# Kernel tuning notes

Measured on AMD Instinct MI355X. Metric: run time of the kernel, lower is better.

The kernel has to match this reference:

```python
import jax, jax.numpy as jnp
import numpy as np

_SAMPLING_EPS = 1e-5


def setup_inputs() -> dict:
    key = jax.random.key(0)
    k1, k2, k3, k4, k5 = jax.random.split(key, 5)
    B, V = 128, 128000
    logits = jax.random.normal(k1, (B, V), dtype=jnp.float32)
    temperature = jax.random.uniform(k2, (B,), dtype=jnp.float32)  # some rows < eps -> greedy
    top_k = jax.random.randint(k3, (B,), 1, 64, dtype=jnp.int32)   # in [1, 63]
    top_p = jax.random.uniform(k4, (B,), dtype=jnp.float32, minval=0.05, maxval=1.0)
    noise_u = jax.random.uniform(k5, (B, V), dtype=jnp.float32, minval=1e-10, maxval=1.0)
    return {"logits": logits, "temperature": temperature, "top_k": top_k,
            "top_p": top_p, "noise_u": noise_u, "max_num_logprobs": 5}


def _apply_top_k_top_p(logits, k, p):
    # Faithful to vLLM: ascending sort, top-k threshold mask, top-p cumsum mask, scatter back.
    B, V = logits.shape
    order = jnp.argsort(logits, axis=-1)                       # ascending, [B, V]
    logits_sort = jnp.take_along_axis(logits, order, axis=-1)
    neg_inf = jnp.float32(-jnp.inf)
    # top-k: pivot value at position V - k; everything strictly below it -> -inf
    pivot_idx = (V - k.astype(jnp.int32))[:, None]             # [B, 1]
    pivot = jnp.take_along_axis(logits_sort, pivot_idx, axis=-1)
    logits_sort = jnp.where(logits_sort < pivot, neg_inf, logits_sort)
    # top-p: softmax over sorted logits, cumsum, drop prefix with mass <= 1 - p (keep last)
    probs_sort = jax.nn.softmax(logits_sort, axis=-1)
    probs_sum = jnp.cumsum(probs_sort, axis=-1)
    top_p_mask = probs_sum <= (1.0 - p)[:, None]
    top_p_mask = top_p_mask.at[:, -1].set(False)
    logits_sort = jnp.where(top_p_mask, neg_inf, logits_sort)
    # scatter back to original vocab order
    rows = jnp.arange(B)[:, None]
    return jnp.zeros_like(logits).at[rows, order].set(logits_sort)


def reference(logits, temperature, top_k, top_p, noise_u, max_num_logprobs):
    # temperature scaling (temp < eps means greedy; divide by 1.0 instead)
    temp = jnp.where(temperature < _SAMPLING_EPS, 1.0, temperature)
    logits = logits.astype(jnp.float32) / temp[:, None]
    # top-k / top-p filtering
    logits = _apply_top_k_top_p(logits, top_k, top_p)
    # probabilities and sampling
    probs = jax.nn.softmax(logits, axis=-1)
    greedy = jnp.argmax(probs, axis=-1)
    q = -jnp.log(noise_u)                                      # Exp(1) noise (q.exponential_())
    random = jnp.argmax(probs / q, axis=-1)
    sampled = jnp.where(temperature < _SAMPLING_EPS, greedy, random).astype(jnp.int32)
    # top-k logprobs
    logprobs = jax.nn.log_softmax(logits, axis=-1)
    topk_logprobs, topk_indices = jax.lax.top_k(logprobs, max_num_logprobs)
    return sampled, topk_indices.astype(jnp.int32), topk_logprobs
```

## Files before the change

### kernel.cpp

```cpp
#include <hip/hip_runtime.h>
#include <math.h>
#include <stdint.h>

#define BT    256
#define NCHUNK 8
#define BINS  2048
#define SHIFT 21
#define TOPC  64
#define CAP2  2048

__device__ __forceinline__ unsigned f2ord(float f) {
    unsigned u = __float_as_uint(f);
    return u ^ ((u & 0x80000000u) ? 0xFFFFFFFFu : 0x80000000u);
}
__device__ __forceinline__ float ord2f(unsigned k) {
    unsigned u = (k & 0x80000000u) ? (k ^ 0x80000000u) : (k ^ 0xFFFFFFFFu);
    return __uint_as_float(u);
}

__global__ __launch_bounds__(BT) void passA_hist(
    const float* __restrict__ logits, unsigned* __restrict__ hist,
    int V, int chunk_len)
{
    __shared__ unsigned h[BINS];
    const int row = blockIdx.y, chunk = blockIdx.x, tid = threadIdx.x;
    const int c0 = chunk * chunk_len;
    int c1 = c0 + chunk_len; if (c1 > V) c1 = V;
    const float* rowp = logits + (size_t)row * (size_t)V;

    for (int i = tid; i < BINS; i += BT) h[i] = 0u;
    __syncthreads();

    for (int base = c0 + tid * 16; base < c1; base += BT * 16) {
        if (base + 16 <= c1) {
            float4 a = *(const float4*)(rowp + base);
            float4 b = *(const float4*)(rowp + base + 4);
            float4 c = *(const float4*)(rowp + base + 8);
            float4 d = *(const float4*)(rowp + base + 12);
            const float v[16] = {a.x,a.y,a.z,a.w, b.x,b.y,b.z,b.w,
                                 c.x,c.y,c.z,c.w, d.x,d.y,d.z,d.w};
            #pragma unroll
            for (int j = 0; j < 16; ++j)
                atomicAdd(&h[f2ord(v[j]) >> SHIFT], 1u);
        } else {
            for (int j = 0; base + j < c1; ++j)
                atomicAdd(&h[f2ord(rowp[base + j]) >> SHIFT], 1u);
        }
    }
    __syncthreads();
    for (int i = tid; i < BINS; i += BT) {
        unsigned v = h[i];
        if (v) atomicAdd(&hist[(size_t)row * BINS + i], v);
    }
}

__global__ __launch_bounds__(BT) void passT_threshold(
    const unsigned* __restrict__ hist, unsigned* __restrict__ thr, int B)
{
    __shared__ unsigned h[BINS];
    __shared__ unsigned seg[BT];
    const int r = blockIdx.x, tid = threadIdx.x;

    for (int i = tid; i < BINS; i += BT) h[i] = hist[(size_t)r * BINS + i];
    __syncthreads();

    unsigned s = 0;
    #pragma unroll
    for (int j = 0; j < BINS / BT; ++j) s += h[tid * (BINS / BT) + j];
    seg[tid] = s;
    __syncthreads();
    for (int off = 1; off < BT; off <<= 1) {
        unsigned v = (tid + off < BT) ? seg[tid + off] : 0u;
        __syncthreads();
        seg[tid] += v;
        __syncthreads();
    }
    unsigned sfx_next = (tid + 1 < BT) ? seg[tid + 1] : 0u;
    if (seg[tid] >= TOPC && sfx_next < TOPC) {
        unsigned running = sfx_next;
        int T = tid * (BINS / BT);
        for (int b = tid * (BINS / BT) + (BINS / BT) - 1; b >= tid * (BINS / BT); --b) {
            running += h[b];
            if (running >= TOPC) { T = b; break; }
        }
        thr[r] = ((unsigned)T) << SHIFT;
    }
}

__global__ __launch_bounds__(BT) void passB_gather(
    const float* __restrict__ logits, const unsigned* __restrict__ thr,
    unsigned* __restrict__ cnt, uint2* __restrict__ cand,
    int V, int chunk_len)
{
    const int row = blockIdx.y, chunk = blockIdx.x, tid = threadIdx.x;
    const int lane = tid & 63;
    const int c0 = chunk * chunk_len;
    int c1 = c0 + chunk_len; if (c1 > V) c1 = V;
    const float* rowp = logits + (size_t)row * (size_t)V;
    const unsigned t = thr[row];

    for (int base = c0 + tid * 16; base < c1; base += BT * 16) {
        unsigned k[16];
        int nval;
        if (base + 16 <= c1) {
            float4 a = *(const float4*)(rowp + base);
            float4 b = *(const float4*)(rowp + base + 4);
            float4 c = *(const float4*)(rowp + base + 8);
            float4 d = *(const float4*)(rowp + base + 12);
            const float v[16] = {a.x,a.y,a.z,a.w, b.x,b.y,b.z,b.w,
                                 c.x,c.y,c.z,c.w, d.x,d.y,d.z,d.w};
            #pragma unroll
            for (int j = 0; j < 16; ++j) k[j] = f2ord(v[j]);
            nval = 16;
        } else {
            nval = c1 - base;
            for (int j = 0; j < nval; ++j) k[j] = f2ord(rowp[base + j]);
        }
        #pragma unroll
        for (int j = 0; j < 16; ++j) {
            bool pass = (j < nval) && (k[j] >= t);
            unsigned long long mask = __ballot(pass);
            if (mask) {
                int leader = __ffsll((unsigned long long)mask) - 1;
                unsigned b0 = 0u;
                if (lane == leader)
                    b0 = atomicAdd(&cnt[row], (unsigned)__popcll(mask));
                b0 = __shfl(b0, leader);
                if (pass) {
                    unsigned pos = b0 + (unsigned)__popcll(mask & ((1ull << lane) - 1ull));
                    if (pos < CAP2)
                        cand[(size_t)row * CAP2 + pos] = make_uint2(k[j], (unsigned)(base + j));
                }
            }
        }
    }
}

__device__ void radix_select_compact(unsigned* s_key, int* s_idx,
                                     unsigned* s_ckey, int* s_cidx,
                                     unsigned* s_hist, unsigned* p_cnt2,
                                     unsigned n, int tid)
{
    unsigned prefix = 0u;
    int remaining = TOPC;
    for (int shift = 28; shift >= 0; shift -= 4) {
        if (tid < 16) s_hist[tid] = 0u;
        __syncthreads();
        for (unsigned i = (unsigned)tid; i < n; i += BT) {
            unsigned k = s_key[i];
            bool ing = (shift == 28) || ((k >> (shift + 4)) == (prefix >> (shift + 4)));
            if (ing) atomicAdd(&s_hist[(k >> shift) & 15u], 1u);
        }
        __syncthreads();
        int cum = 0; int b = 0;
        for (int bb = 15; bb >= 0; --bb) {
            cum += (int)s_hist[bb];
            if (cum >= remaining) { b = bb; break; }
        }
        remaining -= (cum - (int)s_hist[b]);
        prefix |= ((unsigned)b) << shift;
        __syncthreads();
    }
    if (tid == 0) *p_cnt2 = 0u;
    __syncthreads();
    for (unsigned i = (unsigned)tid; i < n; i += BT) {
        unsigned k = s_key[i];
        if (k > prefix) {
            unsigned pos = atomicAdd(p_cnt2, 1u);
            s_ckey[pos] = k; s_cidx[pos] = s_idx[i];
        }
    }
    __syncthreads();
    for (unsigned i = (unsigned)tid; i < n; i += BT) {
        unsigned k = s_key[i];
        if (k == prefix) {
            unsigned pos = atomicAdd(p_cnt2, 1u);
            if (pos < TOPC) { s_ckey[pos] = k; s_cidx[pos] = s_idx[i]; }
        }
    }
    __syncthreads();
}

__global__ __launch_bounds__(BT) void phase2_sample(
    const unsigned* __restrict__ cnt, const uint2* __restrict__ cand,
    const float* __restrict__ temperature,
    const int*   __restrict__ top_k,
    const float* __restrict__ top_p,
    const float* __restrict__ noise_u,
    float* __restrict__ out,
    int B, int V, int M)
{
    __shared__ unsigned key[CAP2];
    __shared__ int      idx[CAP2];
    __shared__ unsigned ckey[TOPC];
    __shared__ int      cidx[TOPC];
    __shared__ unsigned hist16[16];
    __shared__ unsigned cnt2;
    __shared__ float    sval[TOPC], se[TOPC], sq[TOPC];
    __shared__ int      sidx[TOPC];

    const int r = blockIdx.x, tid = threadIdx.x;

    unsigned n = cnt[r];
    if (n > CAP2) n = CAP2;
    for (unsigned i = (unsigned)tid; i < n; i += BT) {
        uint2 c = cand[(size_t)r * CAP2 + i];
        key[i] = c.x; idx[i] = (int)c.y;
    }
    __syncthreads();

    radix_select_compact(key, idx, ckey, cidx, hist16, &cnt2, n, tid);

    for (int kk = 2; kk <= TOPC; kk <<= 1) {
        for (int j = kk >> 1; j > 0; j >>= 1) {
            if (tid < TOPC / 2) {
                int i0 = ((tid & ~(j - 1)) << 1) | (tid & (j - 1));
                int i1 = i0 | j;
                bool up = ((i0 & kk) == 0);
                unsigned ka = ckey[i0], kb = ckey[i1];
                int ia = cidx[i0], ib = cidx[i1];
                bool gt = (ka > kb) || (ka == kb && ia < ib);
                if (gt == up) { ckey[i0] = kb; ckey[i1] = ka; cidx[i0] = ib; cidx[i1] = ia; }
            }
            __syncthreads();
        }
    }

    float temp_orig = temperature[r];
    float temp = (temp_orig < 1e-5f) ? 1.0f : temp_orig;

    if (tid < TOPC) {
        unsigned k = ckey[TOPC - 1 - tid];
        int id = cidx[TOPC - 1 - tid];
        sval[tid] = ord2f(k) / temp;
        sidx[tid] = id;
        float u = noise_u[(size_t)r * (size_t)V + id];
        sq[tid] = -logf(u);
    }
    __syncthreads();
    if (tid < TOPC) se[tid] = expf(sval[tid] - sval[0]);
    __syncthreads();

    if (tid == 0) {
        int k = top_k[r];
        if (k < 1) k = 1; if (k > TOPC) k = TOPC;
        float p = top_p[r];

        float pivot = sval[k - 1];
        int m = k;
        while (m < TOPC && sval[m] >= pivot) ++m;

        float sum = 0.f;
        for (int i = 0; i < m; ++i) sum += se[i];

        float thr1 = 1.0f - p;
        float S = 0.f;
        int f = 1;
        for (int i = m - 1; i >= 1; --i) {
            S += se[i] / sum;
            if (S > thr1) { f = i + 1; break; }
        }

        float sum2 = 0.f;
        for (int i = 0; i < f; ++i) sum2 += se[i];

        int greedy = sidx[0];
        float best = -1.f; int bidx = 0x7fffffff;
        for (int i = 0; i < f; ++i) {
            float ratio = (se[i] / sum2) / sq[i];
            if (ratio > best || (ratio == best && sidx[i] < bidx)) {
                best = ratio; bidx = sidx[i];
            }
        }
        int sampled = (temp_orig < 1e-5f) ? greedy : bidx;

        float lse = logf(sum2);
        out[r] = (float)sampled;
        float* oidx = out + B + (size_t)r * M;
        float* olp  = out + B + (size_t)B * M + (size_t)r * M;
        int produced = 0;
        for (int i = 0; i < f && produced < M; ++i, ++produced) {
            oidx[produced] = (float)sidx[i];
            olp[produced]  = (sval[i] - sval[0]) - lse;
        }
        int v = 0;
        while (produced < M) {
            bool used = false;
            for (int i = 0; i < f; ++i) if (sidx[i] == v) { used = true; break; }
            if (!used) { oidx[produced] = (float)v; olp[produced] = -3.0e38f; ++produced; }
            ++v;
        }
    }
}

extern "C" void kernel_launch(void* const* d_in, const int* in_sizes, int n_in,
                              void* d_out, int out_size, void* d_ws, size_t ws_size,
                              hipStream_t stream)
{
    const float* logits      = (const float*)d_in[0];
    const float* temperature = (const float*)d_in[1];
    const int*   top_k       = (const int*)d_in[2];
    const float* top_p       = (const float*)d_in[3];
    const float* noise_u     = (const float*)d_in[4];

    const int B = in_sizes[1];
    const int V = in_sizes[0] / B;
    const int M = (out_size / B - 1) / 2;

    char* w = (char*)d_ws;
    unsigned* cnt  = (unsigned*)w;
    unsigned* hist = (unsigned*)(w + 1024);
    unsigned* thr  = (unsigned*)(w + 1024 + (size_t)B * BINS * 4);
    uint2*    cand = (uint2*)   (w + 1024 + (size_t)B * BINS * 4 + 1024);

    hipMemsetAsync(d_ws, 0, 1024 + (size_t)B * BINS * 4, stream);

    int chunk_len = (((V + NCHUNK - 1) / NCHUNK) + 15) & ~15;

    dim3 g(NCHUNK, B);
    passA_hist     <<<g, BT, 0, stream>>>(logits, hist, V, chunk_len);
    passT_threshold<<<B, BT, 0, stream>>>(hist, thr, B);
    passB_gather   <<<g, BT, 0, stream>>>(logits, thr, cnt, cand, V, chunk_len);
    phase2_sample  <<<B, BT, 0, stream>>>(cnt, cand, temperature, top_k, top_p,
                                          noise_u, (float*)d_out, B, V, M);
}
```

Baseline: 218.0 us.

## Store per-chunk 16-bit histograms, coalesce loads, and simplify gather filtering

```diff
diff --git a/kernel.cpp b/kernel.cpp
--- a/kernel.cpp
+++ b/kernel.cpp
@@ -2,12 +2,12 @@
 #include <math.h>
 #include <stdint.h>
 
-#define BT    256
+#define BT     256
 #define NCHUNK 8
-#define BINS  2048
-#define SHIFT 21
-#define TOPC  64
-#define CAP2  2048
+#define BINS   1024
+#define SHIFT  22
+#define TOPC   64
+#define CAP2   1024
 
 __device__ __forceinline__ unsigned f2ord(float f) {
     unsigned u = __float_as_uint(f);
@@ -19,7 +19,7 @@
 }
 
 __global__ __launch_bounds__(BT) void passA_hist(
-    const float* __restrict__ logits, unsigned* __restrict__ hist,
+    const float* __restrict__ logits, unsigned short* __restrict__ hist,
     int V, int chunk_len)
 {
     __shared__ unsigned h[BINS];
@@ -31,37 +31,46 @@
     for (int i = tid; i < BINS; i += BT) h[i] = 0u;
     __syncthreads();
 
-    for (int base = c0 + tid * 16; base < c1; base += BT * 16) {
-        if (base + 16 <= c1) {
-            float4 a = *(const float4*)(rowp + base);
-            float4 b = *(const float4*)(rowp + base + 4);
-            float4 c = *(const float4*)(rowp + base + 8);
-            float4 d = *(const float4*)(rowp + base + 12);
-            const float v[16] = {a.x,a.y,a.z,a.w, b.x,b.y,b.z,b.w,
-                                 c.x,c.y,c.z,c.w, d.x,d.y,d.z,d.w};
-            #pragma unroll
-            for (int j = 0; j < 16; ++j)
-                atomicAdd(&h[f2ord(v[j]) >> SHIFT], 1u);
-        } else {
-            for (int j = 0; base + j < c1; ++j)
-                atomicAdd(&h[f2ord(rowp[base + j]) >> SHIFT], 1u);
-        }
-    }
-    __syncthreads();
-    for (int i = tid; i < BINS; i += BT) {
-        unsigned v = h[i];
-        if (v) atomicAdd(&hist[(size_t)row * BINS + i], v);
-    }
+    for (int base = c0; base < c1; base += BT * 16) {
+        #pragma unroll
+        for (int q = 0; q < 4; ++q) {
+            int off = base + q * BT * 4 + tid * 4;
+            if (off + 4 <= c1) {
+                float4 a = *(const float4*)(rowp + off);
+                atomicAdd(&h[f2ord(a.x) >> SHIFT], 1u);
+                atomicAdd(&h[f2ord(a.y) >> SHIFT], 1u);
+                atomicAdd(&h[f2ord(a.z) >> SHIFT], 1u);
+                atomicAdd(&h[f2ord(a.w) >> SHIFT], 1u);
+            } else {
+                for (int j = 0; j < 4; ++j)
+                    if (off + j < c1)
+                        atomicAdd(&h[f2ord(rowp[off + j]) >> SHIFT], 1u);
+            }
+        }
+    }
+    __syncthreads();
+    unsigned* hp = (unsigned*)(hist + ((size_t)row * NCHUNK + chunk) * BINS);
+    for (int p = tid; p < BINS / 2; p += BT)
+        hp[p] = (h[2 * p] & 0xFFFFu) | (h[2 * p + 1] << 16);
 }
 
 __global__ __launch_bounds__(BT) void passT_threshold(
-    const unsigned* __restrict__ hist, unsigned* __restrict__ thr, int B)
+    const unsigned short* __restrict__ hist, unsigned* __restrict__ thr, int B)
 {
     __shared__ unsigned h[BINS];
     __shared__ unsigned seg[BT];
     const int r = blockIdx.x, tid = threadIdx.x;
 
-    for (int i = tid; i < BINS; i += BT) h[i] = hist[(size_t)r * BINS + i];
+    const unsigned* hp = (const unsigned*)(hist + (size_t)r * NCHUNK * BINS);
+    for (int p = tid; p < BINS / 2; p += BT) {
+        unsigned a0 = 0u, a1 = 0u;
+        #pragma unroll
+        for (int c = 0; c < NCHUNK; ++c) {
+            unsigned u = hp[(size_t)c * (BINS / 2) + p];
+            a0 += u & 0xFFFFu; a1 += u >> 16;
+        }
+        h[2 * p] = a0; h[2 * p + 1] = a1;
+    }
     __syncthreads();
 
     unsigned s = 0;
@@ -93,44 +102,38 @@
     int V, int chunk_len)
 {
     const int row = blockIdx.y, chunk = blockIdx.x, tid = threadIdx.x;
-    const int lane = tid & 63;
     const int c0 = chunk * chunk_len;
     int c1 = c0 + chunk_len; if (c1 > V) c1 = V;
     const float* rowp = logits + (size_t)row * (size_t)V;
-    const unsigned t = thr[row];
-
-    for (int base = c0 + tid * 16; base < c1; base += BT * 16) {
-        unsigned k[16];
-        int nval;
-        if (base + 16 <= c1) {
-            float4 a = *(const float4*)(rowp + base);
-            float4 b = *(const float4*)(rowp + base + 4);
-            float4 c = *(const float4*)(rowp + base + 8);
-            float4 d = *(const float4*)(rowp + base + 12);
-            const float v[16] = {a.x,a.y,a.z,a.w, b.x,b.y,b.z,b.w,
-                                 c.x,c.y,c.z,c.w, d.x,d.y,d.z,d.w};
-            #pragma unroll
-            for (int j = 0; j < 16; ++j) k[j] = f2ord(v[j]);
-            nval = 16;
-        } else {
-            nval = c1 - base;
-            for (int j = 0; j < nval; ++j) k[j] = f2ord(rowp[base + j]);
-        }
+    const float tf = ord2f(thr[row]);
+
+    for (int base = c0; base < c1; base += BT * 16) {
         #pragma unroll
-        for (int j = 0; j < 16; ++j) {
-            bool pass = (j < nval) && (k[j] >= t);
-            unsigned long long mask = __ballot(pass);
-            if (mask) {
-                int leader = __ffsll((unsigned long long)mask) - 1;
-                unsigned b0 = 0u;
-                if (lane == leader)
-                    b0 = atomicAdd(&cnt[row], (unsigned)__popcll(mask));
-                b0 = __shfl(b0, leader);
-                if (pass) {
-                    unsigned pos = b0 + (unsigned)__popcll(mask & ((1ull << lane) - 1ull));
-                    if (pos < CAP2)
-                        cand[(size_t)row * CAP2 + pos] = make_uint2(k[j], (unsigned)(base + j));
+        for (int q = 0; q < 4; ++q) {
+            int off = base + q * BT * 4 + tid * 4;
+            if (off + 4 <= c1) {
+                float4 a = *(const float4*)(rowp + off);
+                if (a.x >= tf || a.y >= tf || a.z >= tf || a.w >= tf) {
+                    const float v[4] = {a.x, a.y, a.z, a.w};
+                    for (int j = 0; j < 4; ++j)
+                        if (v[j] >= tf) {
+                            unsigned pos = atomicAdd(&cnt[row], 1u);
+                            if (pos < CAP2)
+                                cand[(size_t)row * CAP2 + pos] =
+                                    make_uint2(f2ord(v[j]), (unsigned)(off + j));
+                        }
                 }
+            } else {
+                for (int j = 0; j < 4; ++j)
+                    if (off + j < c1) {
+                        float v = rowp[off + j];
+                        if (v >= tf) {
+                            unsigned pos = atomicAdd(&cnt[row], 1u);
+                            if (pos < CAP2)
+                                cand[(size_t)row * CAP2 + pos] =
+                                    make_uint2(f2ord(v), (unsigned)(off + j));
+                        }
+                    }
             }
         }
     }
@@ -308,12 +311,12 @@
     const int M = (out_size / B - 1) / 2;
 
     char* w = (char*)d_ws;
-    unsigned* cnt  = (unsigned*)w;
-    unsigned* hist = (unsigned*)(w + 1024);
-    unsigned* thr  = (unsigned*)(w + 1024 + (size_t)B * BINS * 4);
-    uint2*    cand = (uint2*)   (w + 1024 + (size_t)B * BINS * 4 + 1024);
-
-    hipMemsetAsync(d_ws, 0, 1024 + (size_t)B * BINS * 4, stream);
+    unsigned*       cnt  = (unsigned*)w;
+    unsigned*       thr  = (unsigned*)(w + 1024);
+    unsigned short* hist = (unsigned short*)(w + 2048);
+    uint2*          cand = (uint2*)(w + 2048 + (size_t)B * NCHUNK * BINS * 2);
+
+    hipMemsetAsync(d_ws, 0, 1024, stream);
 
     int chunk_len = (((V + NCHUNK - 1) / NCHUNK) + 15) & ~15;
 
```

Result: no change. 218.7 us (+0.3%).
